# Kernel optimization log

Measured on AMD Instinct MI355X. Metric: run time of the kernel, lower is better.

## Reference

```python
import jax, jax.numpy as jnp
import numpy as np

H = 64   # gru_hidden_dim == gnn_hidden_dim
F = 64   # node_feat_dim
K = 8    # k_nn
OUT = 32 # output_factor_dim
BN_EPS = 1e-5


def _gru_scan(x, Wih, Whh, bih, bhh):
    # x: [S, F] single sequence (torch bug makes GRU scan the b*n axis); returns [S, H]
    xp = x @ Wih.T + bih  # [S, 3H], gate order r,z,n (torch convention)
    def step(h, xt):
        hp = h @ Whh.T + bhh
        r = jax.nn.sigmoid(xt[:H] + hp[:H])
        z = jax.nn.sigmoid(xt[H:2 * H] + hp[H:2 * H])
        ng = jnp.tanh(xt[2 * H:] + r * hp[2 * H:])
        hn = (1.0 - z) * ng + z * h
        return hn, hn
    _, out = jax.lax.scan(step, jnp.zeros((H,), x.dtype), xp)
    return out


def _gcn_layer(x, row, col, w, W, b, n):
    # PyG GCNConv: out[col] += d^{-1/2}[row] * w * d^{-1/2}[col] * (x @ W.T)[row] + b
    xw = x @ W.T
    deg = jnp.zeros((n,), x.dtype).at[col].add(w)
    dinv = deg ** -0.5
    dinv = jnp.where(jnp.isinf(dinv), 0.0, dinv)
    norm = dinv[row] * w * dinv[col]
    out = jnp.zeros_like(xw).at[col].add(norm[:, None] * xw[row])
    return out + b


def setup_inputs() -> dict:
    key = jax.random.key(0)
    ks = jax.random.split(key, 20)
    s = 0.08  # ~ torch uniform(-1/sqrt(64), 1/sqrt(64)) scale
    d = {
        'x_seq': jax.random.normal(ks[0], (4, 8, F, 2048), jnp.float32),
        # gru_sim params
        'Wih_s': jax.random.normal(ks[1], (3 * H, F), jnp.float32) * s,
        'Whh_s': jax.random.normal(ks[2], (3 * H, H), jnp.float32) * s,
        'bih_s': jax.random.normal(ks[3], (3 * H,), jnp.float32) * s,
        'bhh_s': jax.random.normal(ks[4], (3 * H,), jnp.float32) * s,
        # gru params
        'Wih': jax.random.normal(ks[5], (3 * H, F), jnp.float32) * s,
        'Whh': jax.random.normal(ks[6], (3 * H, H), jnp.float32) * s,
        'bih': jax.random.normal(ks[7], (3 * H,), jnp.float32) * s,
        'bhh': jax.random.normal(ks[8], (3 * H,), jnp.float32) * s,
        # gcn1 / gcn2 params (GCNConv weight [out,in], bias [out])
        'W1': jax.random.normal(ks[9], (H, H), jnp.float32) * s,
        'b1': jnp.zeros((H,), jnp.float32),
        'W2': jax.random.normal(ks[10], (H, H), jnp.float32) * s,
        'b2': jnp.zeros((H,), jnp.float32),
        # batchnorm affine
        'gamma': jnp.ones((H,), jnp.float32),
        'beta': jnp.zeros((H,), jnp.float32),
        # predictor
        'Wp': jax.random.normal(ks[11], (OUT, H), jnp.float32) * s,
        'bp': jnp.zeros((OUT,), jnp.float32),
    }
    return d


def reference(x_seq, Wih_s, Whh_s, bih_s, bhh_s, Wih, Whh, bih, bhh,
              W1, b1, W2, b2, gamma, beta, Wp, bp):
    b, l, f, n = x_seq.shape
    # torch GRU is batch_first=True but fed [l, b*n, f]: it scans the b*n axis
    # as time and gru_out[-1] keeps only batch item l-1 -> only last time slice used.
    seq = x_seq[:, -1].transpose(0, 2, 1).reshape(b * n, f)  # [b*n, f]
    h = _gru_scan(seq, Wih_s, Whh_s, bih_s, bhh_s).reshape(b, n, H)      # gru_sim
    h_out = _gru_scan(seq, Wih, Whh, bih, bhh).reshape(b, n, H)          # gru

    # dynamic kNN graph from similarity
    sim = jnp.einsum('bni,bmi->bnm', h, h)
    eye = jnp.eye(n, dtype=bool)
    sim = jnp.where(eye[None], jnp.asarray(-1e9, sim.dtype), sim)
    vals, idx = jax.lax.top_k(sim, K)  # [b, n, K], sorted desc like torch.topk

    # edges: n*K knn edges + n unit-weight self loops (outer add_self_loops;
    # GCNConv's add_remaining_self_loops then adds nothing)
    row = jnp.concatenate([jnp.repeat(jnp.arange(n), K), jnp.arange(n)])

    def per_graph(v, ix, x):
        col = jnp.concatenate([ix.reshape(-1), jnp.arange(n)])
        w = jnp.concatenate([v.reshape(-1), jnp.ones((n,), v.dtype)])
        o1 = jax.nn.relu(_gcn_layer(x, row, col, w, W1, b1, n))
        o2 = jax.nn.relu(_gcn_layer(o1, row, col, w, W2, b2, n))
        return o2

    out2 = jax.vmap(per_graph)(vals, idx, h_out)  # [b, n, H]

    # BatchNorm1d (training mode: biased batch stats over b*n rows)
    flat = out2.reshape(b * n, H)
    mu = flat.mean(0)
    var = flat.var(0)
    normed = (flat - mu) / jnp.sqrt(var + BN_EPS) * gamma + beta

    out = normed @ Wp.T + bp
    return out.reshape(b, n, OUT)
```

## Files before the change

### kernel.cpp

```cpp
#include <hip/hip_runtime.h>
#include <hip/hip_bf16.h>

typedef __hip_bfloat16 bf16;

#define NB   4
#define NN   2048
#define NROW 8192
#define HD   64
#define G3   192
#define KNN  8
#define OUTD 32
#define SCHUNK 32
#define SBURN  96
#define NCH    256
#define SCH4   32
#define SBRN4  40
#define NCH4   256
#define TI   4
#define TOPB 256
#define XPR  32
#define SCR  32
#define TKR  16

#define OFF_FLAG  0u
#define OFF_DEG   64u
#define OFF_DINV  8256u
#define OFF_BNS   16448u
#define OFF_BNSQ  16512u
#define OFF_SCALE 16576u
#define OFF_SHIFT 16640u
#define OFF_VALS  16704u
#define OFF_IDX   82240u
#define OFF_A     147776u
#define OFF_C     672064u
#define OFF_XP0   1196352u
#define OFF_XP1   2769216u
#define OFF_END   4342080u

typedef __attribute__((ext_vector_type(8))) short short8v;
typedef __attribute__((ext_vector_type(4))) float f32x4;

__device__ __forceinline__ float sigmoidf_(float x) { return 1.f / (1.f + __expf(-x)); }
__device__ __forceinline__ float tanhf_(float x) {
    float e = __expf(-2.f * fabsf(x));
    float t = (1.f - e) / (1.f + e);
    return copysignf(t, x);
}
__device__ __forceinline__ float ld(const void* p, size_t i, int isbf) {
    return isbf ? __bfloat162float(((const bf16*)p)[i]) : ((const float*)p)[i];
}
__device__ __forceinline__ float bcast(float v, int k) {
    return __int_as_float(__builtin_amdgcn_readlane(__float_as_int(v), k));
}
__device__ __forceinline__ unsigned short bf16rne(float f) {
    unsigned u = __float_as_uint(f);
    return (unsigned short)((u + 0x7FFFu + ((u >> 16) & 1u)) >> 16);
}

__global__ void probe_kernel(const void* __restrict__ gamma, int* __restrict__ flag)
{
    unsigned w = ((const unsigned*)gamma)[0];
    *flag = (w == 0x3F800000u) ? 0 : 1;
}

__global__ __launch_bounds__(384) void xp_kernel(
    const void* __restrict__ x_seq,
    const void* __restrict__ Wih_s, const void* __restrict__ bih_s,
    const void* __restrict__ Wih,   const void* __restrict__ bih,
    float* __restrict__ xp0, float* __restrict__ xp1,
    const int* __restrict__ dtp)
{
    int isbf = *dtp;
    int row0 = blockIdx.x * XPR;
    int b = row0 >> 11, j0 = row0 & 2047;
    int t = threadIdx.x;

    __shared__ __align__(16) float S[XPR * 68];
    for (int idx = t; idx < XPR * HD; idx += 384) {
        int f = idx >> 5, jj = idx & (XPR - 1);
        S[jj * 68 + f] = ld(x_seq, (size_t)((b * 8 + 7) * 64 + f) * 2048 + (j0 + jj), isbf);
    }

    int g = t % G3;
    const void* W  = (t < G3) ? Wih_s : Wih;
    const void* bi = (t < G3) ? bih_s : bih;
    float* o = (t < G3) ? xp0 : xp1;
    float wreg[64];
    #pragma unroll
    for (int k = 0; k < 64; ++k) wreg[k] = ld(W, g * HD + k, isbf);
    float bias = ld(bi, g, isbf);
    __syncthreads();

    for (int jj = 0; jj < XPR; ++jj) {
        const float4* s4 = (const float4*)(S + jj * 68);
        float a0 = bias, a1 = 0.f, a2 = 0.f, a3 = 0.f;
        #pragma unroll
        for (int q = 0; q < 16; ++q) {
            float4 v = s4[q];
            a0 += wreg[4*q+0] * v.x;
            a1 += wreg[4*q+1] * v.y;
            a2 += wreg[4*q+2] * v.z;
            a3 += wreg[4*q+3] * v.w;
        }
        o[(size_t)(row0 + jj) * G3 + g] = (a0 + a1) + (a2 + a3);
    }
}

__global__ __launch_bounds__(128) void gru_scan_pack_kernel(
    const float* __restrict__ xp0, const float* __restrict__ xp1,
    const void* __restrict__ Whh_s, const void* __restrict__ bhh_s,
    const void* __restrict__ Whh,   const void* __restrict__ bhh,
    unsigned short* __restrict__ hAhi, unsigned short* __restrict__ hAlo,
    float* __restrict__ hC,
    const int* __restrict__ dtp)
{
    int isbf = *dtp;
    int gru = blockIdx.x >> 7;
    int pb  = blockIdx.x & 127;
    int w   = threadIdx.x >> 6;
    int L   = threadIdx.x & 63;
    int chunk = pb * 2 + w;
    const float* xpp = gru ? xp1 : xp0;
    const void* Wh   = gru ? Whh : Whh_s;
    const void* bh_p = gru ? bhh : bhh_s;

    __shared__ __align__(16) float4 SW4[64 * 64];

    for (int idx = threadIdx.x; idx < 64 * 64; idx += 128) {
        int k = idx >> 6, j = idx & 63;
        float4 v;
        v.x = ld(Wh, (size_t)j * 64 + k, isbf);
        v.y = ld(Wh, (size_t)(64 + j) * 64 + k, isbf);
        v.z = ld(Wh, (size_t)(128 + j) * 64 + k, isbf);
        v.w = 0.f;
        SW4[idx] = v;
    }
    float br  = ld(bh_p, L, isbf);
    float bz  = ld(bh_p, 64 + L, isbf);
    float bn_ = ld(bh_p, 128 + L, isbf);
    __syncthreads();

    int first = chunk * SCH4;
    int burn  = min(SBRN4, first);
    int start = first - burn;
    int steps = burn + SCH4;

    float hval = 0.f;
    size_t rb = (size_t)start * G3;
    float xr = xpp[rb + L];
    float xz = xpp[rb + 64 + L];
    float xn = xpp[rb + 128 + L];

    for (int t = 0; t < steps; ++t) {
        size_t nb = (size_t)min(start + t + 1, NROW - 1) * G3;
        float pxr = xpp[nb + L];
        float pxz = xpp[nb + 64 + L];
        float pxn = xpp[nb + 128 + L];

        float pr0 = br, pz0 = bz, pn0 = bn_;
        float pr1 = 0.f, pz1 = 0.f, pn1 = 0.f;
        #pragma unroll
        for (int k = 0; k < 64; k += 2) {
            float4 w0 = SW4[k * 64 + L];
            float4 w1 = SW4[(k + 1) * 64 + L];
            float b0 = bcast(hval, k);
            float b1 = bcast(hval, k + 1);
            pr0 += w0.x * b0; pz0 += w0.y * b0; pn0 += w0.z * b0;
            pr1 += w1.x * b1; pz1 += w1.y * b1; pn1 += w1.z * b1;
        }

        float r  = sigmoidf_(xr + pr0 + pr1);
        float z  = sigmoidf_(xz + pz0 + pz1);
        float ng = tanhf_(xn + r * (pn0 + pn1));
        hval = (1.f - z) * ng + z * hval;

        if (t >= burn) {
            size_t o = (size_t)(start + t) * HD + L;
            if (gru) {
                hC[o] = hval;
            } else {
                unsigned short hb = bf16rne(hval);
                float hf = __uint_as_float(((unsigned)hb) << 16);
                hAhi[o] = hb;
                hAlo[o] = bf16rne(hval - hf);
            }
        }
        xr = pxr; xz = pxz; xn = pxn;
    }
}

__global__ __launch_bounds__(192, 2) void gru_scan_fused_kernel(
    const void* __restrict__ x_seq,
    const void* __restrict__ Wih_s, const void* __restrict__ bih_s,
    const void* __restrict__ Whh_s, const void* __restrict__ bhh_s,
    const void* __restrict__ Wih,   const void* __restrict__ bih,
    const void* __restrict__ Whh,   const void* __restrict__ bhh,
    float* __restrict__ hA, float* __restrict__ hC,
    const int* __restrict__ dtp)
{
    int isbf = *dtp;
    int gru   = blockIdx.x >> 8;
    int chunk = blockIdx.x & 255;
    const void* Wh = gru ? Whh : Whh_s;
    const void* bh_p = gru ? bhh : bhh_s;
    const void* Wi = gru ? Wih : Wih_s;
    const void* bi_p = gru ? bih : bih_s;
    float* hout = gru ? hC : hA;

    int lane = threadIdx.x & 63;
    int w    = threadIdx.x >> 6;
    int g    = w * 64 + lane;

    float whh[64], wih[64];
    #pragma unroll
    for (int k = 0; k < 64; ++k) {
        whh[k] = ld(Wh, g * 64 + k, isbf);
        wih[k] = ld(Wi, g * 64 + k, isbf);
    }
    float bh = ld(bh_p, g, isbf);
    float bi = ld(bi_p, g, isbf);

    __shared__ float hs[64];
    __shared__ float ss[64];
    __shared__ float gr[64], gz[64], ga[64], gx[64];

    int first = chunk * SCHUNK;
    int burn  = min(SBURN, first);
    int start = first - burn;
    int steps = burn + SCHUNK;

    #define XIDX(r) ((size_t)((((r) >> 11) * 8 + 7) * 64 + lane) * 2048 + ((r) & 2047))
    float sf = 0.f;
    if (w == 0) {
        ss[lane] = ld(x_seq, XIDX(start), isbf);
        if (steps > 1) sf = ld(x_seq, XIDX(start + 1), isbf);
    }
    __syncthreads();

    float hval = 0.f;
    float sval = ss[lane];

    for (int t = 0; t < steps; ++t) {
        float a = bh, x = bi;
        #pragma unroll
        for (int k = 0; k < 64; ++k) {
            a += whh[k] * bcast(hval, k);
            x += wih[k] * bcast(sval, k);
        }
        if (w == 0)      gr[lane] = sigmoidf_(x + a);
        else if (w == 1) gz[lane] = sigmoidf_(x + a);
        else           { ga[lane] = a; gx[lane] = x; }
        __syncthreads();
        if (w == 0) {
            if (t + 1 < steps) {
                ss[lane] = sf;
                if (t + 2 < steps) sf = ld(x_seq, XIDX(start + t + 2), isbf);
            }
        } else if (w == 2) {
            float hn = (1.f - gz[lane]) * tanhf_(gx[lane] + gr[lane] * ga[lane])
                     + gz[lane] * hval;
            hs[lane] = hn;
            hval = hn;
            if (t >= burn) hout[(size_t)(start + t) * HD + lane] = hn;
        }
        __syncthreads();
        if (w != 2) hval = hs[lane];
        sval = ss[lane];
    }
    #undef XIDX
}

__device__ __forceinline__ void merge8(float tv[KNN], int tj[KNN], int off)
{
    float ov[KNN]; int oj[KNN];
    #pragma unroll
    for (int m = 0; m < KNN; ++m) {
        ov[m] = __shfl_xor(tv[m], off);
        oj[m] = __shfl_xor(tj[m], off);
    }
    #pragma unroll
    for (int m = 0; m < KNN; ++m) {
        if (ov[KNN - 1 - m] > tv[m]) { tv[m] = ov[KNN - 1 - m]; tj[m] = oj[KNN - 1 - m]; }
    }
    #pragma unroll
    for (int d = 4; d > 0; d >>= 1) {
        #pragma unroll
        for (int m = 0; m < KNN; ++m) {
            if ((m & d) == 0 && (m | d) < KNN) {
                int p = m | d;
                if (tv[p] > tv[m]) {
                    float fv = tv[m]; tv[m] = tv[p]; tv[p] = fv;
                    int fj = tj[m]; tj[m] = tj[p]; tj[p] = fj;
                }
            }
        }
    }
}

__global__ __launch_bounds__(256) void topk_mfma_kernel(
    const unsigned short* __restrict__ Ahi, const unsigned short* __restrict__ Alo,
    float* __restrict__ vals, int* __restrict__ idxs, float* __restrict__ deg)
{
    int bid = blockIdx.x;
    int row0 = bid * TKR;
    int bbase = row0 & ~(NN - 1);
    int rloc = row0 & (NN - 1);
    int t = threadIdx.x;
    int w = t >> 6, L = t & 63;
    int cL = L & 15, q = L >> 4;
    int chunk = q * 8;

    __shared__ float mv[4][TKR][KNN];
    __shared__ int   mj[4][TKR][KNN];

    size_t arow = (size_t)(row0 + cL) * HD;
    short8v ahi0 = *(const short8v*)(Ahi + arow + chunk);
    short8v ahi1 = *(const short8v*)(Ahi + arow + 32 + chunk);
    short8v alo0 = *(const short8v*)(Alo + arow + chunk);
    short8v alo1 = *(const short8v*)(Alo + arow + 32 + chunk);

    int jbase = w * 512;

    float tv[4][KNN]; int tj[4][KNN];
    #pragma unroll
    for (int e = 0; e < 4; ++e)
        #pragma unroll
        for (int m = 0; m < KNN; ++m) { tv[e][m] = -3e38f; tj[e][m] = 0; }

    #pragma unroll 1
    for (int strip = 0; strip < 8; ++strip) {
        #pragma unroll
        for (int g = 0; g < 4; ++g) {
            int j0 = jbase + strip * 64 + g * 16;
            size_t brow = (size_t)(bbase + j0 + cL) * HD;
            short8v bhi0 = *(const short8v*)(Ahi + brow + chunk);
            short8v bhi1 = *(const short8v*)(Ahi + brow + 32 + chunk);
            short8v blo0 = *(const short8v*)(Alo + brow + chunk);
            short8v blo1 = *(const short8v*)(Alo + brow + 32 + chunk);
            f32x4 accA = {0.f, 0.f, 0.f, 0.f};
            f32x4 accB = {0.f, 0.f, 0.f, 0.f};
            accA = __builtin_amdgcn_mfma_f32_16x16x32_bf16(ahi0, bhi0, accA, 0, 0, 0);
            accB = __builtin_amdgcn_mfma_f32_16x16x32_bf16(ahi0, blo0, accB, 0, 0, 0);
            accA = __builtin_amdgcn_mfma_f32_16x16x32_bf16(ahi1, bhi1, accA, 0, 0, 0);
            accB = __builtin_amdgcn_mfma_f32_16x16x32_bf16(ahi1, blo1, accB, 0, 0, 0);
            accA = __builtin_amdgcn_mfma_f32_16x16x32_bf16(alo0, bhi0, accA, 0, 0, 0);
            accB = __builtin_amdgcn_mfma_f32_16x16x32_bf16(alo1, bhi1, accB, 0, 0, 0);
            f32x4 acc = accA + accB;
            int jj = j0 + cL;
            #pragma unroll
            for (int e = 0; e < 4; ++e) {
                int r = q * 4 + e;
                float nv = (jj == rloc + r) ? -1e9f : acc[e];
                if (nv > tv[e][KNN - 1]) {
                    tv[e][KNN - 1] = nv; tj[e][KNN - 1] = jj;
                    #pragma unroll
                    for (int m = KNN - 1; m > 0; --m) {
                        if (tv[e][m] > tv[e][m - 1]) {
                            float fv = tv[e][m]; tv[e][m] = tv[e][m - 1]; tv[e][m - 1] = fv;
                            int fj = tj[e][m]; tj[e][m] = tj[e][m - 1]; tj[e][m - 1] = fj;
                        }
                    }
                }
            }
        }
    }

    #pragma unroll
    for (int e = 0; e < 4; ++e) {
        merge8(tv[e], tj[e], 1);
        merge8(tv[e], tj[e], 2);
        merge8(tv[e], tj[e], 4);
        merge8(tv[e], tj[e], 8);
    }
    if (cL == 0) {
        #pragma unroll
        for (int e = 0; e < 4; ++e)
            #pragma unroll
            for (int m = 0; m < KNN; ++m) {
                mv[w][q * 4 + e][m] = tv[e][m];
                mj[w][q * 4 + e][m] = tj[e][m];
            }
    }
    __syncthreads();

    if (w == 0) {
        int r = L >> 2, p = L & 3;
        float fv[KNN]; int fj[KNN];
        #pragma unroll
        for (int m = 0; m < KNN; ++m) { fv[m] = mv[p][r][m]; fj[m] = mj[p][r][m]; }
        merge8(fv, fj, 1);
        merge8(fv, fj, 2);
        if (p == 0) {
            int row = row0 + r;
            #pragma unroll
            for (int m = 0; m < KNN; ++m) {
                vals[(size_t)row * KNN + m] = fv[m];
                idxs[(size_t)row * KNN + m] = fj[m];
                atomicAdd(deg + bbase + fj[m], fv[m]);
            }
            atomicAdd(deg + row, 1.0f);
        }
    }
}

__global__ __launch_bounds__(TOPB, 2) void topk_kernel(
    const float* __restrict__ h,
    float* __restrict__ vals, int* __restrict__ idxs, float* __restrict__ deg)
{
    int bid = blockIdx.x;
    int b    = bid >> 9;
    int row0 = b * NN + (bid & 511) * TI;
    int i0 = row0 & 2047;
    int t = threadIdx.x;

    __shared__ __align__(16) float sim[TI][NN];
    __shared__ __align__(16) float hi[TI * HD];

    for (int q = t; q < TI * HD; q += TOPB)
        hi[q] = h[(size_t)(row0 + (q >> 6)) * HD + (q & 63)];
    __syncthreads();

    const float* hb = h + (size_t)b * NN * HD;
    const float4* hi4 = (const float4*)hi;
    #pragma unroll 1
    for (int j = t; j < NN; j += TOPB) {
        const float4* hr = (const float4*)(hb + (size_t)j * HD);
        float acc[TI];
        #pragma unroll
        for (int m = 0; m < TI; ++m) acc[m] = 0.f;
        #pragma unroll 4
        for (int q = 0; q < 16; ++q) {
            float4 v = hr[q];
            #pragma unroll
            for (int m = 0; m < TI; ++m) {
                float4 c = hi4[m * 16 + q];
                acc[m] += v.x*c.x + v.y*c.y + v.z*c.z + v.w*c.w;
            }
        }
        #pragma unroll
        for (int m = 0; m < TI; ++m)
            sim[m][j] = (j == i0 + m) ? -1e9f : acc[m];
    }
    __syncthreads();

    int w    = t >> 6;
    int lane = t & 63;
    int row  = row0 + w;

    float tv[KNN]; int tj[KNN];
    #pragma unroll
    for (int m = 0; m < KNN; ++m) { tv[m] = -3e38f; tj[m] = 0; }

    for (int k = 0; k < 32; ++k) {
        int j = lane + (k << 6);
        float nv = sim[w][j];
        if (nv > tv[KNN - 1]) {
            tv[KNN - 1] = nv; tj[KNN - 1] = j;
            #pragma unroll
            for (int m = KNN - 1; m > 0; --m) {
                if (tv[m] > tv[m - 1]) {
                    float fv = tv[m]; tv[m] = tv[m - 1]; tv[m - 1] = fv;
                    int fj = tj[m]; tj[m] = tj[m - 1]; tj[m - 1] = fj;
                }
            }
        }
    }

    #pragma unroll
    for (int off = 1; off < 64; off <<= 1) {
        float ov[KNN]; int oj[KNN];
        #pragma unroll
        for (int m = 0; m < KNN; ++m) {
            ov[m] = __shfl_xor(tv[m], off);
            oj[m] = __shfl_xor(tj[m], off);
        }
        #pragma unroll
        for (int m = 0; m < KNN; ++m) {
            if (ov[KNN - 1 - m] > tv[m]) { tv[m] = ov[KNN - 1 - m]; tj[m] = oj[KNN - 1 - m]; }
        }
        if (off < 32) {
            #pragma unroll
            for (int d = 4; d > 0; d >>= 1) {
                #pragma unroll
                for (int m = 0; m < KNN; ++m) {
                    if ((m & d) == 0 && (m | d) < KNN) {
                        int p = m | d;
                        if (tv[p] > tv[m]) {
                            float fv = tv[m]; tv[m] = tv[p]; tv[p] = fv;
                            int fj = tj[m]; tj[m] = tj[p]; tj[p] = fj;
                        }
                    }
                }
            }
        }
    }

    if (lane == 0) {
        #pragma unroll
        for (int m = 0; m < KNN; ++m) {
            vals[(size_t)row * KNN + m] = tv[m];
            idxs[(size_t)row * KNN + m] = tj[m];
            atomicAdd(deg + (b << 11) + tj[m], tv[m]);
        }
        atomicAdd(deg + row, 1.0f);
    }
}

__global__ void dinv_kernel(const float* __restrict__ deg, float* __restrict__ dinv)
{
    int g = blockIdx.x * 256 + threadIdx.x;
    if (g >= NROW) return;
    float d = deg[g];
    float r = 1.f / sqrtf(d);
    dinv[g] = isinf(r) ? 0.f : r;
}

__global__ __launch_bounds__(256) void scatter_kernel(
    const float* __restrict__ in, const void* __restrict__ W,
    const void* __restrict__ bias, int dorelu,
    const float* __restrict__ dinv,
    const float* __restrict__ vals, const int* __restrict__ idxs,
    float* __restrict__ acc, const int* __restrict__ dtp)
{
    int isbf = *dtp;
    int lane = threadIdx.x & 63;
    int w    = threadIdx.x >> 6;

    float wreg[64];
    #pragma unroll
    for (int k = 0; k < 64; ++k) wreg[k] = ld(W, lane * HD + k, isbf);
    float bb = ld(bias, lane, isbf);

    int row0 = blockIdx.x * SCR + w * (SCR / 4);
    #pragma unroll 1
    for (int rr = 0; rr < SCR / 4; ++rr) {
        int row = row0 + rr;
        int b = row >> 11;
        float x = in[(size_t)row * HD + lane];
        if (dorelu) x = fmaxf(x + bb, 0.f);
        float v0 = 0.f, v1 = 0.f, v2 = 0.f, v3 = 0.f;
        #pragma unroll
        for (int k = 0; k < 64; k += 4) {
            v0 += wreg[k]     * bcast(x, k);
            v1 += wreg[k + 1] * bcast(x, k + 1);
            v2 += wreg[k + 2] * bcast(x, k + 2);
            v3 += wreg[k + 3] * bcast(x, k + 3);
        }
        float v = (v0 + v1) + (v2 + v3);
        float di = dinv[row];
        atomicAdd(acc + (size_t)row * HD + lane, di * di * v);
        #pragma unroll
        for (int k = 0; k < KNN; ++k) {
            int c = idxs[(size_t)row * KNN + k];
            float wv = vals[(size_t)row * KNN + k];
            float nw = di * wv * dinv[(b << 11) + c];
            atomicAdd(acc + (size_t)((b << 11) + c) * HD + lane, nw * v);
        }
    }
}

__global__ void bn_stats_kernel(const float* __restrict__ acc2, const void* __restrict__ bias,
                                float* __restrict__ bns, float* __restrict__ bnsq,
                                const int* __restrict__ dtp)
{
    int isbf = *dtp;
    int c = blockIdx.x;
    int t = threadIdx.x;
    float bb = ld(bias, c, isbf);
    float s = 0.f, s2 = 0.f;
    for (int r = t; r < NROW; r += 256) {
        float v = fmaxf(acc2[(size_t)r * HD + c] + bb, 0.f);
        s += v; s2 += v * v;
    }
    __shared__ float sv[4], sv2[4];
    #pragma unroll
    for (int off = 32; off > 0; off >>= 1) {
        s  += __shfl_down(s, off);
        s2 += __shfl_down(s2, off);
    }
    if ((t & 63) == 0) { sv[t >> 6] = s; sv2[t >> 6] = s2; }
    __syncthreads();
    if (t == 0) {
        for (int w = 1; w < 4; ++w) { s += sv[w]; s2 += sv2[w]; }
        bns[c] = s; bnsq[c] = s2;
    }
}

__global__ void bn_final_kernel(const float* __restrict__ bns, const float* __restrict__ bnsq,
                                const void* __restrict__ gamma, const void* __restrict__ beta,
                                float* __restrict__ scale, float* __restrict__ shift,
                                const int* __restrict__ dtp)
{
    int isbf = *dtp;
    int c = threadIdx.x;
    float mu = bns[c] / (float)NROW;
    float var = fmaxf(bnsq[c] / (float)NROW - mu * mu, 0.f);
    float sc = ld(gamma, c, isbf) / sqrtf(var + 1e-5f);
    scale[c] = sc;
    shift[c] = ld(beta, c, isbf) - mu * sc;
}

__global__ void out_kernel(const float* __restrict__ acc2, const void* __restrict__ bias2,
                           const float* __restrict__ scale, const float* __restrict__ shift,
                           const void* __restrict__ Wp, const void* __restrict__ bp,
                           float* __restrict__ out, const int* __restrict__ dtp)
{
    int isbf = *dtp;
    int row0 = blockIdx.x * 2;
    int t = threadIdx.x;
    __shared__ float nl[2 * HD];
    for (int q = t; q < 2 * HD; q += 64) {
        int r = q >> 6, c = q & (HD - 1);
        float v = fmaxf(acc2[(size_t)(row0 + r) * HD + c] + ld(bias2, c, isbf), 0.f);
        nl[q] = v * scale[c] + shift[c];
    }
    __syncthreads();
    int rr = t >> 5, o = t & 31;
    float acc = ld(bp, o, isbf);
    #pragma unroll
    for (int k = 0; k < HD; ++k) acc += nl[rr * HD + k] * ld(Wp, o * HD + k, isbf);
    out[(size_t)(row0 + rr) * OUTD + o] = acc;
}

extern "C" void kernel_launch(void* const* d_in, const int* in_sizes, int n_in,
                              void* d_out, int out_size, void* d_ws, size_t ws_size,
                              hipStream_t stream)
{
    (void)in_sizes; (void)n_in; (void)out_size;
    const void* x_seq = d_in[0];
    const void* Wih_s = d_in[1];
    const void* Whh_s = d_in[2];
    const void* bih_s = d_in[3];
    const void* bhh_s = d_in[4];
    const void* Wih   = d_in[5];
    const void* Whh   = d_in[6];
    const void* bih   = d_in[7];
    const void* bhh   = d_in[8];
    const void* W1    = d_in[9];
    const void* b1    = d_in[10];
    const void* W2    = d_in[11];
    const void* b2    = d_in[12];
    const void* gamma = d_in[13];
    const void* beta  = d_in[14];
    const void* Wp    = d_in[15];
    const void* bp    = d_in[16];
    float* out = (float*)d_out;

    float* ws = (float*)d_ws;
    int*   dtp  = (int*)(ws + OFF_FLAG);
    float* deg  = ws + OFF_DEG;
    float* dinv = ws + OFF_DINV;
    float* bns  = ws + OFF_BNS;
    float* bnsq = ws + OFF_BNSQ;
    float* scale = ws + OFF_SCALE;
    float* shift = ws + OFF_SHIFT;
    float* vals = ws + OFF_VALS;
    int*   idxs = (int*)(ws + OFF_IDX);
    float* A    = ws + OFF_A;
    float* C    = ws + OFF_C;
    float* xp0  = ws + OFF_XP0;
    float* xp1  = ws + OFF_XP1;

    bool big_ws = ws_size >= (size_t)OFF_END * sizeof(float);

    probe_kernel<<<1, 1, 0, stream>>>(gamma, dtp);
    hipMemsetAsync(deg, 0, NROW * sizeof(float), stream);

    if (big_ws) {
        xp_kernel<<<NROW / XPR, 384, 0, stream>>>(x_seq, Wih_s, bih_s, Wih, bih, xp0, xp1, dtp);
        gru_scan_pack_kernel<<<2 * (NCH4 / 2), 128, 0, stream>>>(
            xp0, xp1, Whh_s, bhh_s, Whh, bhh,
            (unsigned short*)A, (unsigned short*)A + (size_t)NROW * HD, C, dtp);
        topk_mfma_kernel<<<NROW / TKR, 256, 0, stream>>>(
            (unsigned short*)A, (unsigned short*)A + (size_t)NROW * HD, vals, idxs, deg);
    } else {
        gru_scan_fused_kernel<<<2 * NCH, 192, 0, stream>>>(x_seq, Wih_s, bih_s, Whh_s, bhh_s,
                                                           Wih, bih, Whh, bhh, A, C, dtp);
        topk_kernel<<<NROW / TI, TOPB, 0, stream>>>(A, vals, idxs, deg);
    }
    dinv_kernel<<<NROW / 256, 256, 0, stream>>>(deg, dinv);

    hipMemsetAsync(A, 0, (size_t)NROW * HD * sizeof(float), stream);
    scatter_kernel<<<NROW / SCR, 256, 0, stream>>>(C, W1, b1, 0, dinv, vals, idxs, A, dtp);

    hipMemsetAsync(C, 0, (size_t)NROW * HD * sizeof(float), stream);
    scatter_kernel<<<NROW / SCR, 256, 0, stream>>>(A, W2, b1, 1, dinv, vals, idxs, C, dtp);

    bn_stats_kernel<<<HD, 256, 0, stream>>>(C, b2, bns, bnsq, dtp);
    bn_final_kernel<<<1, HD, 0, stream>>>(bns, bnsq, gamma, beta, scale, shift, dtp);
    out_kernel<<<NROW / 2, 64, 0, stream>>>(C, b2, scale, shift, Wp, bp, out, dtp);
}
```

Measured before the change: 353.3 us.

## Split top-k column range across 8 waves and parallelize BN stats over rows

The MFMA top-k kernel now launches 512 threads per block, so each of 8 waves scans 256 candidate columns instead of 512. The final merge becomes an 8-way merge done by two waves. The BN statistics kernel now spreads rows across 128 blocks, reading coalesced across the 64 channels and combining partial sums with atomics into buffers that are zeroed beforehand. Both changes aim to raise parallelism and shorten per-thread serial work, at the cost of more merge work, more atomics and a possibly different floating-point summation order.

```diff
diff --git a/kernel.cpp b/kernel.cpp
--- a/kernel.cpp
+++ b/kernel.cpp
@@ -297,7 +297,7 @@
     }
 }
 
-__global__ __launch_bounds__(256) void topk_mfma_kernel(
+__global__ __launch_bounds__(512) void topk_mfma_kernel(
     const unsigned short* __restrict__ Ahi, const unsigned short* __restrict__ Alo,
     float* __restrict__ vals, int* __restrict__ idxs, float* __restrict__ deg)
 {
@@ -310,8 +310,8 @@
     int cL = L & 15, q = L >> 4;
     int chunk = q * 8;
 
-    __shared__ float mv[4][TKR][KNN];
-    __shared__ int   mj[4][TKR][KNN];
+    __shared__ float mv[8][TKR][KNN];
+    __shared__ int   mj[8][TKR][KNN];
 
     size_t arow = (size_t)(row0 + cL) * HD;
     short8v ahi0 = *(const short8v*)(Ahi + arow + chunk);
@@ -319,7 +319,7 @@
     short8v alo0 = *(const short8v*)(Alo + arow + chunk);
     short8v alo1 = *(const short8v*)(Alo + arow + 32 + chunk);
 
-    int jbase = w * 512;
+    int jbase = w * 256;
 
     float tv[4][KNN]; int tj[4][KNN];
     #pragma unroll
@@ -328,7 +328,7 @@
         for (int m = 0; m < KNN; ++m) { tv[e][m] = -3e38f; tj[e][m] = 0; }
 
     #pragma unroll 1
-    for (int strip = 0; strip < 8; ++strip) {
+    for (int strip = 0; strip < 4; ++strip) {
         #pragma unroll
         for (int g = 0; g < 4; ++g) {
             int j0 = jbase + strip * 64 + g * 16;
@@ -383,13 +383,15 @@
     }
     __syncthreads();
 
-    if (w == 0) {
-        int r = L >> 2, p = L & 3;
+    if (w < 2) {
+        int r = (w << 3) + (L >> 3);
+        int p = L & 7;
         float fv[KNN]; int fj[KNN];
         #pragma unroll
         for (int m = 0; m < KNN; ++m) { fv[m] = mv[p][r][m]; fj[m] = mj[p][r][m]; }
         merge8(fv, fj, 1);
         merge8(fv, fj, 2);
+        merge8(fv, fj, 4);
         if (p == 0) {
             int row = row0 + r;
             #pragma unroll
@@ -559,30 +561,30 @@
     }
 }
 
-__global__ void bn_stats_kernel(const float* __restrict__ acc2, const void* __restrict__ bias,
-                                float* __restrict__ bns, float* __restrict__ bnsq,
-                                const int* __restrict__ dtp)
+__global__ __launch_bounds__(256) void bn_stats_kernel(
+    const float* __restrict__ acc2, const void* __restrict__ bias,
+    float* __restrict__ bns, float* __restrict__ bnsq,
+    const int* __restrict__ dtp)
 {
     int isbf = *dtp;
-    int c = blockIdx.x;
-    int t = threadIdx.x;
+    int c  = threadIdx.x & 63;
+    int wv = threadIdx.x >> 6;
+    int row0 = blockIdx.x * 64 + wv * 16;
     float bb = ld(bias, c, isbf);
     float s = 0.f, s2 = 0.f;
-    for (int r = t; r < NROW; r += 256) {
-        float v = fmaxf(acc2[(size_t)r * HD + c] + bb, 0.f);
+    #pragma unroll
+    for (int rr = 0; rr < 16; ++rr) {
+        float v = fmaxf(acc2[(size_t)(row0 + rr) * HD + c] + bb, 0.f);
         s += v; s2 += v * v;
     }
-    __shared__ float sv[4], sv2[4];
-    #pragma unroll
-    for (int off = 32; off > 0; off >>= 1) {
-        s  += __shfl_down(s, off);
-        s2 += __shfl_down(s2, off);
-    }
-    if ((t & 63) == 0) { sv[t >> 6] = s; sv2[t >> 6] = s2; }
-    __syncthreads();
-    if (t == 0) {
-        for (int w = 1; w < 4; ++w) { s += sv[w]; s2 += sv2[w]; }
-        bns[c] = s; bnsq[c] = s2;
+    __shared__ float sv[4][64], sv2[4][64];
+    sv[wv][c] = s; sv2[wv][c] = s2;
+    __syncthreads();
+    if (wv == 0) {
+        s  = sv[0][c] + sv[1][c] + sv[2][c] + sv[3][c];
+        s2 = sv2[0][c] + sv2[1][c] + sv2[2][c] + sv2[3][c];
+        atomicAdd(bns + c, s);
+        atomicAdd(bnsq + c, s2);
     }
 }
 
@@ -665,13 +667,14 @@
 
     probe_kernel<<<1, 1, 0, stream>>>(gamma, dtp);
     hipMemsetAsync(deg, 0, NROW * sizeof(float), stream);
+    hipMemsetAsync(bns, 0, 2 * HD * sizeof(float), stream);
 
     if (big_ws) {
         xp_kernel<<<NROW / XPR, 384, 0, stream>>>(x_seq, Wih_s, bih_s, Wih, bih, xp0, xp1, dtp);
         gru_scan_pack_kernel<<<2 * (NCH4 / 2), 128, 0, stream>>>(
             xp0, xp1, Whh_s, bhh_s, Whh, bhh,
             (unsigned short*)A, (unsigned short*)A + (size_t)NROW * HD, C, dtp);
-        topk_mfma_kernel<<<NROW / TKR, 256, 0, stream>>>(
+        topk_mfma_kernel<<<NROW / TKR, 512, 0, stream>>>(
             (unsigned short*)A, (unsigned short*)A + (size_t)NROW * HD, vals, idxs, deg);
     } else {
         gru_scan_fused_kernel<<<2 * NCH, 192, 0, stream>>>(x_seq, Wih_s, bih_s, Whh_s, bhh_s,
@@ -686,7 +689,7 @@
     hipMemsetAsync(C, 0, (size_t)NROW * HD * sizeof(float), stream);
     scatter_kernel<<<NROW / SCR, 256, 0, stream>>>(A, W2, b1, 1, dinv, vals, idxs, C, dtp);
 
-    bn_stats_kernel<<<HD, 256, 0, stream>>>(C, b2, bns, bnsq, dtp);
+    bn_stats_kernel<<<NROW / 64, 256, 0, stream>>>(C, b2, bns, bnsq, dtp);
     bn_final_kernel<<<1, HD, 0, stream>>>(bns, bnsq, gamma, beta, scale, shift, dtp);
     out_kernel<<<NROW / 2, 64, 0, stream>>>(C, b2, scale, shift, Wp, bp, out, dtp);
 }
```

Result: faster. 342.5 us (-3.1%).
